# Kernel optimization log

Measured on AMD Instinct MI355X. Metric: run time of the kernel, lower is better.

## Reference

```python
import jax, jax.numpy as jnp
import numpy as np

N_NODES = 20000
N_EDGES = 640000
D = 64        # node / edge feature dim
H = 128       # MLP hidden dim


def setup_inputs() -> dict:
    key = jax.random.key(0)
    ks = jax.random.split(key, 12)
    inp = {
        "x": jax.random.normal(ks[0], (N_NODES, D), dtype=jnp.float32),
        "edge_index": jax.random.randint(ks[1], (2, N_EDGES), 0, N_NODES, dtype=jnp.int64),
        "edge_attr": jax.random.normal(ks[2], (N_EDGES, D), dtype=jnp.float32),
        "f": jax.random.normal(ks[3], (N_NODES, D), dtype=jnp.float32),
        # edge MLP: concat(x_src, x_dest, edge_attr) = 3D -> H -> D
        "We1": jax.random.normal(ks[4], (3 * D, H), dtype=jnp.float32) / np.sqrt(3 * D),
        "be1": jnp.zeros((H,), dtype=jnp.float32),
        "We2": jax.random.normal(ks[5], (H, D), dtype=jnp.float32) / np.sqrt(H),
        "be2": jnp.zeros((D,), dtype=jnp.float32),
        # node MLP: concat(x, agg, f) = 3D -> H -> D
        "Wn1": jax.random.normal(ks[6], (3 * D, H), dtype=jnp.float32) / np.sqrt(3 * D),
        "bn1": jnp.zeros((H,), dtype=jnp.float32),
        "Wn2": jax.random.normal(ks[7], (H, D), dtype=jnp.float32) / np.sqrt(H),
        "bn2": jnp.zeros((D,), dtype=jnp.float32),
    }
    return inp


def reference(x, edge_index, edge_attr, f, We1, be1, We2, be2, Wn1, bn1, Wn2, bn2):
    src, dest = edge_index[0], edge_index[1]
    # edge model: MLP over gathered src/dest node features + edge attrs
    e_in = jnp.concatenate([x[src], x[dest], edge_attr], axis=-1)      # [E, 3D]
    e_h = jax.nn.relu(e_in @ We1 + be1)                                 # [E, H]
    edge_out = e_h @ We2 + be2                                          # [E, D]
    # node model: scatter-add edge messages to dest, then MLP
    agg = jax.ops.segment_sum(edge_out, dest, num_segments=N_NODES)    # [N, D]
    n_in = jnp.concatenate([x, agg, f], axis=-1)                        # [N, 3D]
    n_h = jax.nn.relu(n_in @ Wn1 + bn1)                                 # [N, H]
    x_out = n_h @ Wn2 + bn2                                             # [N, D]
    return (x_out, edge_out)
```

## Files before the change

kernel.cpp:

```cpp
#include <hip/hip_runtime.h>

#define NE 640000
#define NN 20000
#define SEI 200
#define SEH 136
#define SEO 68

typedef __attribute__((ext_vector_type(8))) short s16x8;
typedef __attribute__((ext_vector_type(4))) short s16x4;
typedef __attribute__((ext_vector_type(4))) float f32x4;

typedef const __attribute__((ext_vector_type(4))) float cf32x4;

__device__ __forceinline__ short f2bf(float f) {
  unsigned int u = __float_as_uint(f);
  u += 0x7fffu + ((u >> 16) & 1u);
  return (short)(u >> 16);
}

__device__ __forceinline__ s16x8 cvt8(f32x4 a, f32x4 b) {
  s16x8 o;
  o[0]=f2bf(a[0]); o[1]=f2bf(a[1]); o[2]=f2bf(a[2]); o[3]=f2bf(a[3]);
  o[4]=f2bf(b[0]); o[5]=f2bf(b[1]); o[6]=f2bf(b[2]); o[7]=f2bf(b[3]);
  return o;
}

__device__ __forceinline__ void load_wfrags_lds(const float* W1, const float* W2,
                                                const float* b1, const float* b2,
                                                short* smem, int t,
                                                int wv, int r, int g,
                                                s16x8 w1f[2][6], s16x8 w2f[4],
                                                f32x4 b1r[2], f32x4* b2r) {
  #pragma unroll
  for (int i = 0; i < 24; ++i) {
    int idx4 = t + i * 256;
    f32x4 v = ((cf32x4*)W1)[idx4];
    s16x4 pk; pk[0]=f2bf(v[0]); pk[1]=f2bf(v[1]); pk[2]=f2bf(v[2]); pk[3]=f2bf(v[3]);
    *(s16x4*)&smem[idx4 * 4] = pk;
  }
  __syncthreads();
  #pragma unroll
  for (int nn = 0; nn < 2; ++nn) {
    const int h = (wv*2+nn)*16 + r;
    #pragma unroll
    for (int kk = 0; kk < 6; ++kk) {
      s16x8 wf;
      #pragma unroll
      for (int i = 0; i < 8; ++i) wf[i] = smem[(kk*32 + g*8 + i)*128 + h];
      w1f[nn][kk] = wf;
    }
    b1r[nn] = *(cf32x4*)(b1 + (wv*2+nn)*16 + g*4);
  }
  __syncthreads();
  #pragma unroll
  for (int i = 0; i < 8; ++i) {
    int idx4 = t + i * 256;
    f32x4 v = ((cf32x4*)W2)[idx4];
    s16x4 pk; pk[0]=f2bf(v[0]); pk[1]=f2bf(v[1]); pk[2]=f2bf(v[2]); pk[3]=f2bf(v[3]);
    *(s16x4*)&smem[idx4 * 4] = pk;
  }
  __syncthreads();
  {
    const int h2 = wv*16 + r;
    #pragma unroll
    for (int kk = 0; kk < 4; ++kk) {
      s16x8 wf;
      #pragma unroll
      for (int i = 0; i < 8; ++i) wf[i] = smem[(kk*32 + g*8 + i)*64 + h2];
      w2f[kk] = wf;
    }
    *b2r = *(cf32x4*)(b2 + wv*16 + g*4);
  }
  __syncthreads();
}


__global__ void count_kernel(const int* __restrict__ eidx, int* __restrict__ cursor) {
  for (int e = blockIdx.x * blockDim.x + threadIdx.x; e < NE;
       e += gridDim.x * blockDim.x)
    atomicAdd(&cursor[eidx[NE + e]], 1);
}

__global__ __launch_bounds__(1024)
void scan_kernel(int* __restrict__ cursor, int* __restrict__ offs) {
  __shared__ int part[1024];
  const int t = threadIdx.x;
  const int CH = 20;
  const int lo = t * CH, hi = min(lo + CH, NN);
  int s = 0;
  for (int i = lo; i < hi; ++i) s += cursor[i];
  part[t] = s;
  __syncthreads();
  for (int d = 1; d < 1024; d <<= 1) {
    int u = (t >= d) ? part[t - d] : 0;
    __syncthreads();
    part[t] += u;
    __syncthreads();
  }
  int run = part[t] - s;
  for (int i = lo; i < hi; ++i) {
    int c = cursor[i];
    offs[i] = run;
    cursor[i] = run;
    run += c;
  }
  if (t == 1023) offs[NN] = NE;
}

__global__ void scatter_kernel(const int* __restrict__ eidx,
                               int* __restrict__ cursor, int* __restrict__ elist) {
  for (int e = blockIdx.x * blockDim.x + threadIdx.x; e < NE;
       e += gridDim.x * blockDim.x) {
    int pos = atomicAdd(&cursor[eidx[NE + e]], 1);
    elist[pos] = e;
  }
}

#define LOAD_ROWS(sv, dv, ee) do {                                        \
    cf32x4* ps_ = (cf32x4*)(x  + (size_t)(sv)*64 + p*16);                 \
    cf32x4* pd_ = (cf32x4*)(x  + (size_t)(dv)*64 + p*16);                 \
    cf32x4* pe_ = (cf32x4*)(ea + (size_t)(ee)*64 + p*16);                 \
    L[0]=ps_[0]; L[1]=ps_[1]; L[2]=ps_[2];  L[3]=ps_[3];                  \
    L[4]=pd_[0]; L[5]=pd_[1]; L[6]=pd_[2];  L[7]=pd_[3];                  \
    L[8]=pe_[0]; L[9]=pe_[1]; L[10]=pe_[2]; L[11]=pe_[3];                 \
  } while (0)

#define WRITE_EIN(buf) do {                                               \
    short* stg_ = (buf) + el*SEI + p*16;                                  \
    ((s16x8*)stg_)[0]       = cvt8(L[0], L[1]);                           \
    ((s16x8*)stg_)[1]       = cvt8(L[2], L[3]);                           \
    ((s16x8*)(stg_+64))[0]  = cvt8(L[4], L[5]);                           \
    ((s16x8*)(stg_+64))[1]  = cvt8(L[6], L[7]);                           \
    ((s16x8*)(stg_+128))[0] = cvt8(L[8], L[9]);                           \
    ((s16x8*)(stg_+128))[1] = cvt8(L[10], L[11]);                         \
  } while (0)

__global__ __launch_bounds__(256, 2)
void edge_kernel(const float* __restrict__ x, const int* __restrict__ eidx,
                 const float* __restrict__ ea, const int* __restrict__ elist,
                 const float* __restrict__ We1, const float* __restrict__ be1,
                 const float* __restrict__ We2, const float* __restrict__ be2,
                 float* __restrict__ edge_out, float* __restrict__ agg)
{
  __shared__ __align__(16) char smem[69632];
  short* sEin0 = (short*)smem;
  short* sEin1 = (short*)(smem + 25600);
  short* sEh   = (short*)(smem + 51200);
  float* fEout = (float*)(smem + 51200);
  int* sDest0  = (int*)(smem + 68608);
  int* sDest1  = (int*)(smem + 68864);
  int* sEid0   = (int*)(smem + 69120);
  int* sEid1   = (int*)(smem + 69376);

  const int t = threadIdx.x;
  const int wv = t >> 6, lane = t & 63;
  const int r = lane & 15, g = lane >> 4;

  s16x8 w1f[2][6], w2f[4];
  f32x4 b1r[2], b2r;
  load_wfrags_lds(We1, We2, be1, be2, (short*)smem, t, wv, r, g,
                  w1f, w2f, b1r, &b2r);

  const int el = t >> 2, p = t & 3;
  const int nT = NE / 64;
  const int S = (int)gridDim.x;
  const f32x4 zero = {0.f, 0.f, 0.f, 0.f};

  f32x4 L[12];
  int eW = 0, dW = 0;
  int eI = 0, sI = 0, dI = 0;
  int tile = blockIdx.x;

  if (tile < nT) {
    int e0 = elist[(tile << 6) + el];
    int s0 = eidx[e0], d0 = eidx[NE + e0];
    LOAD_ROWS(s0, d0, e0);
    WRITE_EIN(sEin0);
    if (p == 0) { sDest0[el] = d0; sEid0[el] = e0; }
    const int t1 = tile + S;
    if (t1 < nT) {
      eW = elist[(t1 << 6) + el];
      int sv = eidx[eW]; dW = eidx[NE + eW];
      LOAD_ROWS(sv, dW, eW);
    }
    const int t2 = tile + 2 * S;
    if (t2 < nT) {
      eI = elist[(t2 << 6) + el];
      sI = eidx[eI]; dI = eidx[NE + eI];
    }
  }
  __syncthreads();

  int cur = 0;
  while (tile < nT) {
    const short* Ecur = cur ? sEin1 : sEin0;
    short* Enxt = cur ? sEin0 : sEin1;
    const int* sDestC = cur ? sDest1 : sDest0;
    const int* sEidC  = cur ? sEid1  : sEid0;
    int* sDestN = cur ? sDest0 : sDest1;
    int* sEidN  = cur ? sEid0  : sEid1;

    const int tW = tile + S, tI = tile + 2 * S, tX = tile + 3 * S;
    if (tW < nT) {
      WRITE_EIN(Enxt);
      if (p == 0) { sDestN[el] = dW; sEidN[el] = eW; }
    }
    if (tI < nT) { LOAD_ROWS(sI, dI, eI); eW = eI; dW = dI; }
    if (tX < nT) {
      eI = elist[(tX << 6) + el];
      sI = eidx[eI]; dI = eidx[NE + eI];
    }

    f32x4 acc1[2][4];
    #pragma unroll
    for (int nn = 0; nn < 2; ++nn)
      #pragma unroll
      for (int j = 0; j < 4; ++j) acc1[nn][j] = zero;
    #pragma unroll
    for (int kk = 0; kk < 6; ++kk) {
      #pragma unroll
      for (int j = 0; j < 4; ++j) {
        s16x8 ef = *(const s16x8*)&Ecur[(j*16 + r)*SEI + kk*32 + g*8];
        acc1[0][j] = __builtin_amdgcn_mfma_f32_16x16x32_bf16(w1f[0][kk], ef, acc1[0][j], 0, 0, 0);
        acc1[1][j] = __builtin_amdgcn_mfma_f32_16x16x32_bf16(w1f[1][kk], ef, acc1[1][j], 0, 0, 0);
      }
    }
    #pragma unroll
    for (int nn = 0; nn < 2; ++nn)
      #pragma unroll
      for (int j = 0; j < 4; ++j) {
        s16x4 pk;
        #pragma unroll
        for (int q = 0; q < 4; ++q) {
          float v = acc1[nn][j][q] + b1r[nn][q];
          pk[q] = f2bf(v > 0.f ? v : 0.f);
        }
        *(s16x4*)&sEh[(j*16 + r)*SEH + (wv*2+nn)*16 + g*4] = pk;
      }
    __syncthreads();

    f32x4 a2s[4];
    #pragma unroll
    for (int j = 0; j < 4; ++j) {
      f32x4 a2 = zero;
      #pragma unroll
      for (int kk = 0; kk < 4; ++kk) {
        s16x8 hf = *(const s16x8*)&sEh[(j*16 + r)*SEH + kk*32 + g*8];
        a2 = __builtin_amdgcn_mfma_f32_16x16x32_bf16(w2f[kk], hf, a2, 0, 0, 0);
      }
      a2 += b2r;
      a2s[j] = a2;
      const int eg = sEidC[j*16 + r];
      *(f32x4*)&edge_out[(size_t)eg*64 + wv*16 + g*4] = a2;
    }
    __syncthreads();

    #pragma unroll
    for (int j = 0; j < 4; ++j)
      *(f32x4*)&fEout[(j*16 + r)*SEO + wv*16 + g*4] = a2s[j];
    __syncthreads();

    {
      const int row0 = wv * 16;
      float acc = fEout[row0*SEO + lane];
      int dcur = sDestC[row0];
      #pragma unroll
      for (int k = 1; k < 16; ++k) {
        const int dn = sDestC[row0 + k];
        const float v = fEout[(row0 + k)*SEO + lane];
        if (dn != dcur) {
          unsafeAtomicAdd(&agg[(size_t)dcur*64 + lane], acc);
          acc = v; dcur = dn;
        } else {
          acc += v;
        }
      }
      unsafeAtomicAdd(&agg[(size_t)dcur*64 + lane], acc);
    }
    __syncthreads();
    cur ^= 1;
    tile += S;
  }
}

__global__ __launch_bounds__(256, 2)
void node_kernel(const float* __restrict__ x, const float* agg,
                 const float* __restrict__ f,
                 const float* __restrict__ Wn1, const float* __restrict__ bn1,
                 const float* __restrict__ Wn2, const float* __restrict__ bn2,
                 float* x_out)
{
  __shared__ __align__(16) char smem[49152];
  short* sEin = (short*)smem;
  short* sEh  = (short*)(smem + 25600);

  const int t = threadIdx.x;
  const int wv = t >> 6, lane = t & 63;
  const int r = lane & 15, g = lane >> 4;

  s16x8 w1f[2][6], w2f[4];
  f32x4 b1r[2], b2r;
  load_wfrags_lds(Wn1, Wn2, bn1, bn2, (short*)smem, t, wv, r, g,
                  w1f, w2f, b1r, &b2r);

  const int el = t >> 2, p = t & 3;
  const f32x4 zero = {0.f, 0.f, 0.f, 0.f};
  const int base = blockIdx.x << 6;
  const int i = base + el;

  f32x4 L[12];
  if (i < NN) {
    cf32x4* ps_ = (cf32x4*)(x   + (size_t)i*64 + p*16);
    cf32x4* pa_ = (cf32x4*)(agg + (size_t)i*64 + p*16);
    cf32x4* pf_ = (cf32x4*)(f   + (size_t)i*64 + p*16);
    L[0]=ps_[0]; L[1]=ps_[1]; L[2]=ps_[2];  L[3]=ps_[3];
    L[4]=pa_[0]; L[5]=pa_[1]; L[6]=pa_[2];  L[7]=pa_[3];
    L[8]=pf_[0]; L[9]=pf_[1]; L[10]=pf_[2]; L[11]=pf_[3];
  } else {
    #pragma unroll
    for (int q = 0; q < 12; ++q) L[q] = zero;
  }
  WRITE_EIN(sEin);
  __syncthreads();

  f32x4 acc1[2][4];
  #pragma unroll
  for (int nn = 0; nn < 2; ++nn)
    #pragma unroll
    for (int j = 0; j < 4; ++j) acc1[nn][j] = zero;
  #pragma unroll
  for (int kk = 0; kk < 6; ++kk) {
    #pragma unroll
    for (int j = 0; j < 4; ++j) {
      s16x8 ef = *(const s16x8*)&sEin[(j*16 + r)*SEI + kk*32 + g*8];
      acc1[0][j] = __builtin_amdgcn_mfma_f32_16x16x32_bf16(w1f[0][kk], ef, acc1[0][j], 0, 0, 0);
      acc1[1][j] = __builtin_amdgcn_mfma_f32_16x16x32_bf16(w1f[1][kk], ef, acc1[1][j], 0, 0, 0);
    }
  }
  #pragma unroll
  for (int nn = 0; nn < 2; ++nn)
    #pragma unroll
    for (int j = 0; j < 4; ++j) {
      s16x4 pk;
      #pragma unroll
      for (int q = 0; q < 4; ++q) {
        float v = acc1[nn][j][q] + b1r[nn][q];
        pk[q] = f2bf(v > 0.f ? v : 0.f);
      }
      *(s16x4*)&sEh[(j*16 + r)*SEH + (wv*2+nn)*16 + g*4] = pk;
    }
  __syncthreads();

  #pragma unroll
  for (int j = 0; j < 4; ++j) {
    f32x4 a2 = zero;
    #pragma unroll
    for (int kk = 0; kk < 4; ++kk) {
      s16x8 hf = *(const s16x8*)&sEh[(j*16 + r)*SEH + kk*32 + g*8];
      a2 = __builtin_amdgcn_mfma_f32_16x16x32_bf16(w2f[kk], hf, a2, 0, 0, 0);
    }
    const int row = base + j*16 + r;
    if (row < NN) {
      f32x4 v = a2 + b2r;
      *(f32x4*)&x_out[(size_t)row*64 + wv*16 + g*4] = v;
    }
  }
}

extern "C" void kernel_launch(void* const* d_in, const int* in_sizes, int n_in,
                              void* d_out, int out_size, void* d_ws, size_t ws_size,
                              hipStream_t stream) {
  const float* x   = (const float*)d_in[0];
  const int*   ei  = (const int*)d_in[1];
  const float* ea  = (const float*)d_in[2];
  const float* f   = (const float*)d_in[3];
  const float* We1 = (const float*)d_in[4];
  const float* be1 = (const float*)d_in[5];
  const float* We2 = (const float*)d_in[6];
  const float* be2 = (const float*)d_in[7];
  const float* Wn1 = (const float*)d_in[8];
  const float* bn1 = (const float*)d_in[9];
  const float* Wn2 = (const float*)d_in[10];
  const float* bn2 = (const float*)d_in[11];

  float* x_out    = (float*)d_out;
  float* edge_out = x_out + (size_t)NN * 64;

  int* cursor = (int*)d_ws;
  int* offs   = cursor + NN;
  int* elist  = offs + NN + 8;

  hipMemsetAsync(x_out, 0, (size_t)NN * 64 * sizeof(float), stream);
  hipMemsetAsync(cursor, 0, NN * sizeof(int), stream);
  count_kernel<<<1024, 256, 0, stream>>>(ei, cursor);
  scan_kernel<<<1, 1024, 0, stream>>>(cursor, offs);
  scatter_kernel<<<1024, 256, 0, stream>>>(ei, cursor, elist);
  edge_kernel<<<512, 256, 0, stream>>>(x, ei, ea, elist, We1, be1, We2, be2,
                                       edge_out, x_out);
  node_kernel<<<313, 256, 0, stream>>>(x, x_out, f, Wn1, bn1, Wn2, bn2, x_out);
}
```

Measured before the change: 250.1 us.

## Vectorize CSR build, stage scan in LDS, reuse edge buffer, persist node kernel

The count and scatter kernels now read four destination indices per thread with int4 loads, using exact-sized grids. The scan kernel stages counts in shared memory so the serial per-thread loops do not hit global memory, and writes results back coalesced. The edge kernel writes its fp32 output directly into the now-free current input buffer, which removes one barrier and the register staging. The node kernel becomes a grid-stride loop over 105 blocks so the weight-fragment load is amortised across tiles, at the cost of fewer concurrent blocks.

```diff
diff --git a/kernel.cpp b/kernel.cpp
--- a/kernel.cpp
+++ b/kernel.cpp
@@ -76,19 +76,29 @@
 
 
 __global__ void count_kernel(const int* __restrict__ eidx, int* __restrict__ cursor) {
-  for (int e = blockIdx.x * blockDim.x + threadIdx.x; e < NE;
-       e += gridDim.x * blockDim.x)
-    atomicAdd(&cursor[eidx[NE + e]], 1);
+  const int4* d4 = (const int4*)(eidx + NE);
+  int i = blockIdx.x * blockDim.x + threadIdx.x;
+  if (i < NE / 4) {
+    int4 d = d4[i];
+    atomicAdd(&cursor[d.x], 1);
+    atomicAdd(&cursor[d.y], 1);
+    atomicAdd(&cursor[d.z], 1);
+    atomicAdd(&cursor[d.w], 1);
+  }
 }
 
 __global__ __launch_bounds__(1024)
 void scan_kernel(int* __restrict__ cursor, int* __restrict__ offs) {
+  __shared__ int cnt[20480];
   __shared__ int part[1024];
   const int t = threadIdx.x;
-  const int CH = 20;
-  const int lo = t * CH, hi = min(lo + CH, NN);
+  for (int i = t; i < 20480; i += 1024)
+    cnt[i] = (i < NN) ? cursor[i] : 0;
+  __syncthreads();
+  const int lo = t * 20;
   int s = 0;
-  for (int i = lo; i < hi; ++i) s += cursor[i];
+  #pragma unroll
+  for (int k = 0; k < 20; ++k) s += cnt[lo + k];
   part[t] = s;
   __syncthreads();
   for (int d = 1; d < 1024; d <<= 1) {
@@ -98,21 +108,32 @@
     __syncthreads();
   }
   int run = part[t] - s;
-  for (int i = lo; i < hi; ++i) {
-    int c = cursor[i];
-    offs[i] = run;
-    cursor[i] = run;
+  #pragma unroll
+  for (int k = 0; k < 20; ++k) {
+    int c = cnt[lo + k];
+    cnt[lo + k] = run;
     run += c;
+  }
+  __syncthreads();
+  for (int i = t; i < NN; i += 1024) {
+    int v = cnt[i];
+    offs[i] = v;
+    cursor[i] = v;
   }
   if (t == 1023) offs[NN] = NE;
 }
 
 __global__ void scatter_kernel(const int* __restrict__ eidx,
                                int* __restrict__ cursor, int* __restrict__ elist) {
-  for (int e = blockIdx.x * blockDim.x + threadIdx.x; e < NE;
-       e += gridDim.x * blockDim.x) {
-    int pos = atomicAdd(&cursor[eidx[NE + e]], 1);
-    elist[pos] = e;
+  const int4* d4 = (const int4*)(eidx + NE);
+  int i = blockIdx.x * blockDim.x + threadIdx.x;
+  if (i < NE / 4) {
+    int4 d = d4[i];
+    const int e = i * 4;
+    elist[atomicAdd(&cursor[d.x], 1)] = e;
+    elist[atomicAdd(&cursor[d.y], 1)] = e + 1;
+    elist[atomicAdd(&cursor[d.z], 1)] = e + 2;
+    elist[atomicAdd(&cursor[d.w], 1)] = e + 3;
   }
 }
 
@@ -146,7 +167,6 @@
   short* sEin0 = (short*)smem;
   short* sEin1 = (short*)(smem + 25600);
   short* sEh   = (short*)(smem + 51200);
-  float* fEout = (float*)(smem + 51200);
   int* sDest0  = (int*)(smem + 68608);
   int* sDest1  = (int*)(smem + 68864);
   int* sEid0   = (int*)(smem + 69120);
@@ -195,6 +215,7 @@
   while (tile < nT) {
     const short* Ecur = cur ? sEin1 : sEin0;
     short* Enxt = cur ? sEin0 : sEin1;
+    float* EoutC = (float*)(cur ? (smem + 25600) : smem);
     const int* sDestC = cur ? sDest1 : sDest0;
     const int* sEidC  = cur ? sEid1  : sEid0;
     int* sDestN = cur ? sDest0 : sDest1;
@@ -239,7 +260,6 @@
       }
     __syncthreads();
 
-    f32x4 a2s[4];
     #pragma unroll
     for (int j = 0; j < 4; ++j) {
       f32x4 a2 = zero;
@@ -249,25 +269,20 @@
         a2 = __builtin_amdgcn_mfma_f32_16x16x32_bf16(w2f[kk], hf, a2, 0, 0, 0);
       }
       a2 += b2r;
-      a2s[j] = a2;
       const int eg = sEidC[j*16 + r];
       *(f32x4*)&edge_out[(size_t)eg*64 + wv*16 + g*4] = a2;
-    }
-    __syncthreads();
-
-    #pragma unroll
-    for (int j = 0; j < 4; ++j)
-      *(f32x4*)&fEout[(j*16 + r)*SEO + wv*16 + g*4] = a2s[j];
+      *(f32x4*)&EoutC[(j*16 + r)*SEO + wv*16 + g*4] = a2;
+    }
     __syncthreads();
 
     {
       const int row0 = wv * 16;
-      float acc = fEout[row0*SEO + lane];
+      float acc = EoutC[row0*SEO + lane];
       int dcur = sDestC[row0];
       #pragma unroll
       for (int k = 1; k < 16; ++k) {
         const int dn = sDestC[row0 + k];
-        const float v = fEout[(row0 + k)*SEO + lane];
+        const float v = EoutC[(row0 + k)*SEO + lane];
         if (dn != dcur) {
           unsafeAtomicAdd(&agg[(size_t)dcur*64 + lane], acc);
           acc = v; dcur = dn;
@@ -305,64 +320,68 @@
 
   const int el = t >> 2, p = t & 3;
   const f32x4 zero = {0.f, 0.f, 0.f, 0.f};
-  const int base = blockIdx.x << 6;
-  const int i = base + el;
-
-  f32x4 L[12];
-  if (i < NN) {
-    cf32x4* ps_ = (cf32x4*)(x   + (size_t)i*64 + p*16);
-    cf32x4* pa_ = (cf32x4*)(agg + (size_t)i*64 + p*16);
-    cf32x4* pf_ = (cf32x4*)(f   + (size_t)i*64 + p*16);
-    L[0]=ps_[0]; L[1]=ps_[1]; L[2]=ps_[2];  L[3]=ps_[3];
-    L[4]=pa_[0]; L[5]=pa_[1]; L[6]=pa_[2];  L[7]=pa_[3];
-    L[8]=pf_[0]; L[9]=pf_[1]; L[10]=pf_[2]; L[11]=pf_[3];
-  } else {
-    #pragma unroll
-    for (int q = 0; q < 12; ++q) L[q] = zero;
-  }
-  WRITE_EIN(sEin);
-  __syncthreads();
-
-  f32x4 acc1[2][4];
-  #pragma unroll
-  for (int nn = 0; nn < 2; ++nn)
-    #pragma unroll
-    for (int j = 0; j < 4; ++j) acc1[nn][j] = zero;
-  #pragma unroll
-  for (int kk = 0; kk < 6; ++kk) {
+  const int nT = (NN + 63) / 64;
+
+  for (int tile = blockIdx.x; tile < nT; tile += (int)gridDim.x) {
+    const int base = tile << 6;
+    const int i = base + el;
+
+    f32x4 L[12];
+    if (i < NN) {
+      cf32x4* ps_ = (cf32x4*)(x   + (size_t)i*64 + p*16);
+      cf32x4* pa_ = (cf32x4*)(agg + (size_t)i*64 + p*16);
+      cf32x4* pf_ = (cf32x4*)(f   + (size_t)i*64 + p*16);
+      L[0]=ps_[0]; L[1]=ps_[1]; L[2]=ps_[2];  L[3]=ps_[3];
+      L[4]=pa_[0]; L[5]=pa_[1]; L[6]=pa_[2];  L[7]=pa_[3];
+      L[8]=pf_[0]; L[9]=pf_[1]; L[10]=pf_[2]; L[11]=pf_[3];
+    } else {
+      #pragma unroll
+      for (int q = 0; q < 12; ++q) L[q] = zero;
+    }
+    WRITE_EIN(sEin);
+    __syncthreads();
+
+    f32x4 acc1[2][4];
+    #pragma unroll
+    for (int nn = 0; nn < 2; ++nn)
+      #pragma unroll
+      for (int j = 0; j < 4; ++j) acc1[nn][j] = zero;
+    #pragma unroll
+    for (int kk = 0; kk < 6; ++kk) {
+      #pragma unroll
+      for (int j = 0; j < 4; ++j) {
+        s16x8 ef = *(const s16x8*)&sEin[(j*16 + r)*SEI + kk*32 + g*8];
+        acc1[0][j] = __builtin_amdgcn_mfma_f32_16x16x32_bf16(w1f[0][kk], ef, acc1[0][j], 0, 0, 0);
+        acc1[1][j] = __builtin_amdgcn_mfma_f32_16x16x32_bf16(w1f[1][kk], ef, acc1[1][j], 0, 0, 0);
+      }
+    }
+    #pragma unroll
+    for (int nn = 0; nn < 2; ++nn)
+      #pragma unroll
+      for (int j = 0; j < 4; ++j) {
+        s16x4 pk;
+        #pragma unroll
+        for (int q = 0; q < 4; ++q) {
+          float v = acc1[nn][j][q] + b1r[nn][q];
+          pk[q] = f2bf(v > 0.f ? v : 0.f);
+        }
+        *(s16x4*)&sEh[(j*16 + r)*SEH + (wv*2+nn)*16 + g*4] = pk;
+      }
+    __syncthreads();
+
     #pragma unroll
     for (int j = 0; j < 4; ++j) {
-      s16x8 ef = *(const s16x8*)&sEin[(j*16 + r)*SEI + kk*32 + g*8];
-      acc1[0][j] = __builtin_amdgcn_mfma_f32_16x16x32_bf16(w1f[0][kk], ef, acc1[0][j], 0, 0, 0);
-      acc1[1][j] = __builtin_amdgcn_mfma_f32_16x16x32_bf16(w1f[1][kk], ef, acc1[1][j], 0, 0, 0);
-    }
-  }
-  #pragma unroll
-  for (int nn = 0; nn < 2; ++nn)
-    #pragma unroll
-    for (int j = 0; j < 4; ++j) {
-      s16x4 pk;
-      #pragma unroll
-      for (int q = 0; q < 4; ++q) {
-        float v = acc1[nn][j][q] + b1r[nn][q];
-        pk[q] = f2bf(v > 0.f ? v : 0.f);
-      }
-      *(s16x4*)&sEh[(j*16 + r)*SEH + (wv*2+nn)*16 + g*4] = pk;
-    }
-  __syncthreads();
-
-  #pragma unroll
-  for (int j = 0; j < 4; ++j) {
-    f32x4 a2 = zero;
-    #pragma unroll
-    for (int kk = 0; kk < 4; ++kk) {
-      s16x8 hf = *(const s16x8*)&sEh[(j*16 + r)*SEH + kk*32 + g*8];
-      a2 = __builtin_amdgcn_mfma_f32_16x16x32_bf16(w2f[kk], hf, a2, 0, 0, 0);
-    }
-    const int row = base + j*16 + r;
-    if (row < NN) {
-      f32x4 v = a2 + b2r;
-      *(f32x4*)&x_out[(size_t)row*64 + wv*16 + g*4] = v;
+      f32x4 a2 = zero;
+      #pragma unroll
+      for (int kk = 0; kk < 4; ++kk) {
+        s16x8 hf = *(const s16x8*)&sEh[(j*16 + r)*SEH + kk*32 + g*8];
+        a2 = __builtin_amdgcn_mfma_f32_16x16x32_bf16(w2f[kk], hf, a2, 0, 0, 0);
+      }
+      const int row = base + j*16 + r;
+      if (row < NN) {
+        f32x4 v = a2 + b2r;
+        *(f32x4*)&x_out[(size_t)row*64 + wv*16 + g*4] = v;
+      }
     }
   }
 }
@@ -392,10 +411,10 @@
 
   hipMemsetAsync(x_out, 0, (size_t)NN * 64 * sizeof(float), stream);
   hipMemsetAsync(cursor, 0, NN * sizeof(int), stream);
-  count_kernel<<<1024, 256, 0, stream>>>(ei, cursor);
+  count_kernel<<<625, 256, 0, stream>>>(ei, cursor);
   scan_kernel<<<1, 1024, 0, stream>>>(cursor, offs);
-  scatter_kernel<<<1024, 256, 0, stream>>>(ei, cursor, elist);
+  scatter_kernel<<<625, 256, 0, stream>>>(ei, cursor, elist);
   edge_kernel<<<512, 256, 0, stream>>>(x, ei, ea, elist, We1, be1, We2, be2,
                                        edge_out, x_out);
-  node_kernel<<<313, 256, 0, stream>>>(x, x_out, f, Wn1, bn1, Wn2, bn2, x_out);
-}
+  node_kernel<<<105, 256, 0, stream>>>(x, x_out, f, Wn1, bn1, Wn2, bn2, x_out);
+}
```

New measurement: 227.1 us. -9.2%, faster.
